# Optimization experiments

Measured on AMD Instinct MI355X. Metric: run time of the kernel, lower is better.

## Reference

```python
import jax, jax.numpy as jnp
import numpy as np
from jax import lax

TAGSET = 48
START_TAG = 46
STOP_TAG = 47
B, T = 128, 256

def setup_inputs() -> dict:
    key = jax.random.key(0)
    k1, k2, k3 = jax.random.split(key, 3)
    features = jax.random.normal(k1, (B, T, TAGSET, TAGSET), dtype=jnp.float32)
    targets = jax.random.randint(k2, (B, T), 0, TAGSET * TAGSET, dtype=jnp.int64)
    # lengths in [1, T], sorted descending as pack_padded_sequence expects
    lengths = jnp.sort(jax.random.randint(k3, (B,), 1, T + 1, dtype=jnp.int64))[::-1]
    return {"features": features, "targets": targets, "lengths": lengths}

def reference(features, targets, lengths):
    b, t, k, _ = features.shape
    # gold score: gather flattened (from_tag*K + to_tag) scores, sum over valid timesteps
    gathered = jnp.take_along_axis(
        features.reshape(b, t, k * k), targets[..., None], axis=2
    ).squeeze(-1)  # (B, T)
    valid = jnp.arange(t)[None, :] < lengths[:, None]  # (B, T) bool
    gold_score = jnp.sum(jnp.where(valid, gathered, 0.0))

    # forward algorithm: t=0 initializes from START_TAG row (all lengths >= 1)
    init = features[:, 0, START_TAG, :]  # (B, K)

    def step(scores_upto_t, inputs):
        feats_t, mask_t = inputs  # (B, K, K), (B,)
        upd = jax.nn.logsumexp(feats_t + scores_upto_t[:, :, None], axis=1)  # lse over from-tag
        new = jnp.where(mask_t[:, None], upd, scores_upto_t)  # freeze finished sequences
        return new, None

    feats_rest = jnp.swapaxes(features[:, 1:], 0, 1)  # (T-1, B, K, K)
    mask_rest = jnp.swapaxes(valid[:, 1:], 0, 1)      # (T-1, B)
    final, _ = lax.scan(step, init, (feats_rest, mask_rest))
    all_paths_scores = final[:, STOP_TAG].sum()
    return all_paths_scores - gold_score
```

## Files before the change

kernel.cpp:

```cpp
#include <hip/hip_runtime.h>


#define NB 128
#define NT 256
#define NK 48
#define NKK (NK * NK)
#define TAG_START 46
#define TAG_STOP 47
#define K_LOG2E 1.4426950408889634f
#define K_LN2   0.6931471805599453f

#define DECL48(v) \
  float v##0,v##1,v##2,v##3,v##4,v##5,v##6,v##7,v##8,v##9,v##10,v##11, \
        v##12,v##13,v##14,v##15,v##16,v##17,v##18,v##19,v##20,v##21,v##22,v##23, \
        v##24,v##25,v##26,v##27,v##28,v##29,v##30,v##31,v##32,v##33,v##34,v##35, \
        v##36,v##37,v##38,v##39,v##40,v##41,v##42,v##43,v##44,v##45,v##46,v##47;

#define LD48C(v, p) \
  v##0 =(p)[0*NK];  v##1 =(p)[1*NK];  v##2 =(p)[2*NK];  v##3 =(p)[3*NK]; \
  v##4 =(p)[4*NK];  v##5 =(p)[5*NK];  v##6 =(p)[6*NK];  v##7 =(p)[7*NK]; \
  v##8 =(p)[8*NK];  v##9 =(p)[9*NK];  v##10=(p)[10*NK]; v##11=(p)[11*NK]; \
  v##12=(p)[12*NK]; v##13=(p)[13*NK]; v##14=(p)[14*NK]; v##15=(p)[15*NK]; \
  v##16=(p)[16*NK]; v##17=(p)[17*NK]; v##18=(p)[18*NK]; v##19=(p)[19*NK]; \
  v##20=(p)[20*NK]; v##21=(p)[21*NK]; v##22=(p)[22*NK]; v##23=(p)[23*NK]; \
  v##24=(p)[24*NK]; v##25=(p)[25*NK]; v##26=(p)[26*NK]; v##27=(p)[27*NK]; \
  v##28=(p)[28*NK]; v##29=(p)[29*NK]; v##30=(p)[30*NK]; v##31=(p)[31*NK]; \
  v##32=(p)[32*NK]; v##33=(p)[33*NK]; v##34=(p)[34*NK]; v##35=(p)[35*NK]; \
  v##36=(p)[36*NK]; v##37=(p)[37*NK]; v##38=(p)[38*NK]; v##39=(p)[39*NK]; \
  v##40=(p)[40*NK]; v##41=(p)[41*NK]; v##42=(p)[42*NK]; v##43=(p)[43*NK]; \
  v##44=(p)[44*NK]; v##45=(p)[45*NK]; v##46=(p)[46*NK]; v##47=(p)[47*NK];

#define LD48R(v, p) { \
  const float4* q_ = (const float4*)(p); \
  float4 r0_=q_[0], r1_=q_[1], r2_ =q_[2],  r3_ =q_[3]; \
  float4 r4_=q_[4], r5_=q_[5], r6_ =q_[6],  r7_ =q_[7]; \
  float4 r8_=q_[8], r9_=q_[9], r10_=q_[10], r11_=q_[11]; \
  v##0 =r0_.x;  v##1 =r0_.y;  v##2 =r0_.z;  v##3 =r0_.w; \
  v##4 =r1_.x;  v##5 =r1_.y;  v##6 =r1_.z;  v##7 =r1_.w; \
  v##8 =r2_.x;  v##9 =r2_.y;  v##10=r2_.z;  v##11=r2_.w; \
  v##12=r3_.x;  v##13=r3_.y;  v##14=r3_.z;  v##15=r3_.w; \
  v##16=r4_.x;  v##17=r4_.y;  v##18=r4_.z;  v##19=r4_.w; \
  v##20=r5_.x;  v##21=r5_.y;  v##22=r5_.z;  v##23=r5_.w; \
  v##24=r6_.x;  v##25=r6_.y;  v##26=r6_.z;  v##27=r6_.w; \
  v##28=r7_.x;  v##29=r7_.y;  v##30=r7_.z;  v##31=r7_.w; \
  v##32=r8_.x;  v##33=r8_.y;  v##34=r8_.z;  v##35=r8_.w; \
  v##36=r9_.x;  v##37=r9_.y;  v##38=r9_.z;  v##39=r9_.w; \
  v##40=r10_.x; v##41=r10_.y; v##42=r10_.z; v##43=r10_.w; \
  v##44=r11_.x; v##45=r11_.y; v##46=r11_.z; v##47=r11_.w; }

#define RL(i) __int_as_float(__builtin_amdgcn_readlane(__float_as_int(s2), (i)))
#define TT(v,i) exp2f(__builtin_fmaf(v##i, K_LOG2E, RL(i)))

#define SUMTREE48(v) \
 ((((((TT(v,0)+TT(v,1))+(TT(v,2)+TT(v,3)))+((TT(v,4)+TT(v,5))+(TT(v,6)+TT(v,7)))) + \
    (((TT(v,8)+TT(v,9))+(TT(v,10)+TT(v,11)))+((TT(v,12)+TT(v,13))+(TT(v,14)+TT(v,15))))) + \
   ((((TT(v,16)+TT(v,17))+(TT(v,18)+TT(v,19)))+((TT(v,20)+TT(v,21))+(TT(v,22)+TT(v,23)))) + \
    (((TT(v,24)+TT(v,25))+(TT(v,26)+TT(v,27)))+((TT(v,28)+TT(v,29))+(TT(v,30)+TT(v,31)))))) + \
  ((((TT(v,32)+TT(v,33))+(TT(v,34)+TT(v,35)))+((TT(v,36)+TT(v,37))+(TT(v,38)+TT(v,39)))) + \
   (((TT(v,40)+TT(v,41))+(TT(v,42)+TT(v,43)))+((TT(v,44)+TT(v,45))+(TT(v,46)+TT(v,47))))))

#define STEP48(v, LDM) { \
  float acc_ = SUMTREE48(v); \
  { int up_ = u + 3; if (up_ > nsteps) up_ = nsteps; \
    const float* p_ = basep + (long)up_ * dstep; LDM(v, p_) } \
  float l2_ = __log2f(acc_); \
  float d2_ = __int_as_float(__builtin_amdgcn_readfirstlane(__float_as_int(l2_))); \
  s2 = l2_ - d2_; \
  c  = __builtin_fmaf(d2_, K_LN2, c); \
}

#define CHAIN48(LDM) { \
  DECL48(A) DECL48(B) DECL48(C) \
  { const float* p_ = basep + dstep; LDM(A, p_) } \
  { int up_ = (2 > nsteps) ? nsteps : 2; \
    const float* p_ = basep + (long)up_ * dstep; LDM(B, p_) } \
  { int up_ = (3 > nsteps) ? nsteps : 3; \
    const float* p_ = basep + (long)up_ * dstep; LDM(C, p_) } \
  int u = 1; \
  for (;;) { \
    STEP48(A, LDM) if (++u > nsteps) break; \
    STEP48(B, LDM) if (++u > nsteps) break; \
    STEP48(C, LDM) if (++u > nsteps) break; \
  } \
}

__global__ __launch_bounds__(64, 1)
void viterbi_chain_kernel(const float* __restrict__ feats,
                          const int* __restrict__ targets,
                          const int* __restrict__ lengths,
                          float* __restrict__ out,
                          float* __restrict__ ws)
{
    const int bu   = blockIdx.x;
    const int b    = bu >> 1;
    const int dir  = bu & 1;
    const int lane = threadIdx.x;
    const int len = lengths[b], last = len - 1, m = last >> 1;
    const float* __restrict__ fb = feats + (size_t)b * (NT * NKK);

    float gold = 0.f;
    {
        int t   = dir ? (m + 1 + lane) : lane;
        int tmx = dir ? last : m;
        while (t <= tmx) { gold += fb[(size_t)t * NKK + targets[b * NT + t]]; t += 64; }
        #pragma unroll
        for (int o = 32; o; o >>= 1) gold += __shfl_down(gold, o, 64);
    }

    const int ooc = (lane < NK) ? lane : (NK - 1);
    int nsteps = dir ? (last - 1 - m) : m;
    if (nsteps < 0) nsteps = 0;

    float s2, c = 0.f;
    if (dir) s2 = (last == 0) ? ((ooc == TAG_STOP) ? 0.f : -1e30f)
                              : fb[(size_t)last * NKK + (size_t)ooc * NK + TAG_STOP] * K_LOG2E;
    else     s2 = fb[TAG_START * NK + ooc] * K_LOG2E;

    if (nsteps > 0) {
        if (dir) {
            const float* basep = fb + (size_t)last * NKK + (size_t)ooc * NK;
            const long dstep = -(long)NKK;
            CHAIN48(LD48R)
        } else {
            const float* basep = fb + ooc;
            const long dstep = (long)NKK;
            CHAIN48(LD48C)
        }
    }

    if (lane < NK) ws[(size_t)bu * 64 + lane] = s2 * K_LN2;
    if (lane == 0) {
        ws[(size_t)bu * 64 + 48] = c;
        atomicAdd(out, -gold);
    }
}

__global__ __launch_bounds__(64, 1)
void viterbi_combine_kernel(const float* __restrict__ ws,
                            float* __restrict__ out)
{
    const int b = blockIdx.x, lane = threadIdx.x;
    const float* f = ws + (size_t)(2 * b) * 64;
    const float* g = ws + (size_t)(2 * b + 1) * 64;
    float v = -3.0e38f;
    if (lane < NK) v = f[lane] + g[lane];
    float mm = v;
    #pragma unroll
    for (int o = 32; o; o >>= 1) mm = fmaxf(mm, __shfl_xor(mm, o, 64));
    float e = (lane < NK) ? __expf(v - mm) : 0.f;
    #pragma unroll
    for (int o = 32; o; o >>= 1) e += __shfl_xor(e, o, 64);
    if (lane == 0) atomicAdd(out, __logf(e) + mm + f[NK] + g[NK]);
}

extern "C" void kernel_launch(void* const* d_in, const int* in_sizes, int n_in,
                              void* d_out, int out_size, void* d_ws, size_t ws_size,
                              hipStream_t stream) {
    const float* feats   = (const float*)d_in[0];
    const int*   targets = (const int*)d_in[1];
    const int*   lengths = (const int*)d_in[2];
    float*       out     = (float*)d_out;
    float*       ws      = (float*)d_ws;

    hipMemsetAsync(out, 0, sizeof(float), stream);
    viterbi_chain_kernel<<<dim3(2 * NB), dim3(64), 0, stream>>>(feats, targets, lengths, out, ws);
    viterbi_combine_kernel<<<dim3(NB), dim3(64), 0, stream>>>(ws, out);
}
```

Measured before the change: 506.9 us.

## Stage forward-direction step matrices through LDS with coalesced float4 loads

In the forward chain, each lane used to load a strided column of 48 floats per step. Now the whole wave loads each 48x48 step matrix with coalesced float4 loads, prefetched several steps ahead in registers, and writes it into a double-buffered shared-memory tile. The logsumexp then reads its column from LDS. The change also adds scheduling barriers and swaps exp2f for the AMDGCN exp2 builtin. This aims to cut uncoalesced global traffic, but LDS writes and reads now sit on the serial critical path of each step, and there is no explicit barrier between writing and reading the tile (a single wave, so it is likely safe).

```diff
diff --git a/kernel.cpp b/kernel.cpp
--- a/kernel.cpp
+++ b/kernel.cpp
@@ -10,25 +10,21 @@
 #define K_LOG2E 1.4426950408889634f
 #define K_LN2   0.6931471805599453f
 
+#if __has_builtin(__builtin_amdgcn_exp2f)
+#define EXP2(x) __builtin_amdgcn_exp2f(x)
+#else
+#define EXP2(x) exp2f(x)
+#endif
+
+#define SB() __builtin_amdgcn_sched_barrier(0)
+
+#define RL(i) __int_as_float(__builtin_amdgcn_readlane(__float_as_int(s2), (i)))
+
 #define DECL48(v) \
   float v##0,v##1,v##2,v##3,v##4,v##5,v##6,v##7,v##8,v##9,v##10,v##11, \
         v##12,v##13,v##14,v##15,v##16,v##17,v##18,v##19,v##20,v##21,v##22,v##23, \
         v##24,v##25,v##26,v##27,v##28,v##29,v##30,v##31,v##32,v##33,v##34,v##35, \
         v##36,v##37,v##38,v##39,v##40,v##41,v##42,v##43,v##44,v##45,v##46,v##47;
-
-#define LD48C(v, p) \
-  v##0 =(p)[0*NK];  v##1 =(p)[1*NK];  v##2 =(p)[2*NK];  v##3 =(p)[3*NK]; \
-  v##4 =(p)[4*NK];  v##5 =(p)[5*NK];  v##6 =(p)[6*NK];  v##7 =(p)[7*NK]; \
-  v##8 =(p)[8*NK];  v##9 =(p)[9*NK];  v##10=(p)[10*NK]; v##11=(p)[11*NK]; \
-  v##12=(p)[12*NK]; v##13=(p)[13*NK]; v##14=(p)[14*NK]; v##15=(p)[15*NK]; \
-  v##16=(p)[16*NK]; v##17=(p)[17*NK]; v##18=(p)[18*NK]; v##19=(p)[19*NK]; \
-  v##20=(p)[20*NK]; v##21=(p)[21*NK]; v##22=(p)[22*NK]; v##23=(p)[23*NK]; \
-  v##24=(p)[24*NK]; v##25=(p)[25*NK]; v##26=(p)[26*NK]; v##27=(p)[27*NK]; \
-  v##28=(p)[28*NK]; v##29=(p)[29*NK]; v##30=(p)[30*NK]; v##31=(p)[31*NK]; \
-  v##32=(p)[32*NK]; v##33=(p)[33*NK]; v##34=(p)[34*NK]; v##35=(p)[35*NK]; \
-  v##36=(p)[36*NK]; v##37=(p)[37*NK]; v##38=(p)[38*NK]; v##39=(p)[39*NK]; \
-  v##40=(p)[40*NK]; v##41=(p)[41*NK]; v##42=(p)[42*NK]; v##43=(p)[43*NK]; \
-  v##44=(p)[44*NK]; v##45=(p)[45*NK]; v##46=(p)[46*NK]; v##47=(p)[47*NK];
 
 #define LD48R(v, p) { \
   const float4* q_ = (const float4*)(p); \
@@ -48,8 +44,7 @@
   v##40=r10_.x; v##41=r10_.y; v##42=r10_.z; v##43=r10_.w; \
   v##44=r11_.x; v##45=r11_.y; v##46=r11_.z; v##47=r11_.w; }
 
-#define RL(i) __int_as_float(__builtin_amdgcn_readlane(__float_as_int(s2), (i)))
-#define TT(v,i) exp2f(__builtin_fmaf(v##i, K_LOG2E, RL(i)))
+#define TT(v,i) EXP2(__builtin_fmaf(v##i, vlog2e, RL(i)))
 
 #define SUMTREE48(v) \
  ((((((TT(v,0)+TT(v,1))+(TT(v,2)+TT(v,3)))+((TT(v,4)+TT(v,5))+(TT(v,6)+TT(v,7)))) + \
@@ -59,29 +54,66 @@
   ((((TT(v,32)+TT(v,33))+(TT(v,34)+TT(v,35)))+((TT(v,36)+TT(v,37))+(TT(v,38)+TT(v,39)))) + \
    (((TT(v,40)+TT(v,41))+(TT(v,42)+TT(v,43)))+((TT(v,44)+TT(v,45))+(TT(v,46)+TT(v,47))))))
 
-#define STEP48(v, LDM) { \
+#define STEPB(v) { \
   float acc_ = SUMTREE48(v); \
   { int up_ = u + 3; if (up_ > nsteps) up_ = nsteps; \
-    const float* p_ = basep + (long)up_ * dstep; LDM(v, p_) } \
+    const float* p_ = basep + (long)up_ * dstep; LD48R(v, p_) } \
+  SB(); \
   float l2_ = __log2f(acc_); \
   float d2_ = __int_as_float(__builtin_amdgcn_readfirstlane(__float_as_int(l2_))); \
   s2 = l2_ - d2_; \
   c  = __builtin_fmaf(d2_, K_LN2, c); \
 }
 
-#define CHAIN48(LDM) { \
+#define CHAINB() { \
   DECL48(A) DECL48(B) DECL48(C) \
-  { const float* p_ = basep + dstep; LDM(A, p_) } \
+  { const float* p_ = basep + dstep; LD48R(A, p_) } \
   { int up_ = (2 > nsteps) ? nsteps : 2; \
-    const float* p_ = basep + (long)up_ * dstep; LDM(B, p_) } \
+    const float* p_ = basep + (long)up_ * dstep; LD48R(B, p_) } \
   { int up_ = (3 > nsteps) ? nsteps : 3; \
-    const float* p_ = basep + (long)up_ * dstep; LDM(C, p_) } \
+    const float* p_ = basep + (long)up_ * dstep; LD48R(C, p_) } \
   int u = 1; \
   for (;;) { \
-    STEP48(A, LDM) if (++u > nsteps) break; \
-    STEP48(B, LDM) if (++u > nsteps) break; \
-    STEP48(C, LDM) if (++u > nsteps) break; \
+    STEPB(A) if (++u > nsteps) break; \
+    STEPB(B) if (++u > nsteps) break; \
+    STEPB(C) if (++u > nsteps) break; \
   } \
+}
+
+#define DECL9(R) float4 R##0,R##1,R##2,R##3,R##4,R##5,R##6,R##7,R##8;
+
+#define GLD9(R, base) { const float4* q_ = (const float4*)(base); \
+  R##0=q_[lane];     R##1=q_[lane+64];  R##2=q_[lane+128]; \
+  R##3=q_[lane+192]; R##4=q_[lane+256]; R##5=q_[lane+320]; \
+  R##6=q_[lane+384]; R##7=q_[lane+448]; R##8=q_[lane+512]; }
+
+#define WRT9(R, tb) { float4* w_ = (float4*)(tb); \
+  w_[lane]=R##0;     w_[lane+64]=R##1;  w_[lane+128]=R##2; \
+  w_[lane+192]=R##3; w_[lane+256]=R##4; w_[lane+320]=R##5; \
+  w_[lane+384]=R##6; w_[lane+448]=R##7; w_[lane+512]=R##8; }
+
+#define FT(TBR,k) EXP2(__builtin_fmaf(TBF[TBR][k][jc], vlog2e, RL(k)))
+
+#define FSUM(TBR) \
+ ((((((FT(TBR,0)+FT(TBR,1))+(FT(TBR,2)+FT(TBR,3)))+((FT(TBR,4)+FT(TBR,5))+(FT(TBR,6)+FT(TBR,7)))) + \
+    (((FT(TBR,8)+FT(TBR,9))+(FT(TBR,10)+FT(TBR,11)))+((FT(TBR,12)+FT(TBR,13))+(FT(TBR,14)+FT(TBR,15))))) + \
+   ((((FT(TBR,16)+FT(TBR,17))+(FT(TBR,18)+FT(TBR,19)))+((FT(TBR,20)+FT(TBR,21))+(FT(TBR,22)+FT(TBR,23)))) + \
+    (((FT(TBR,24)+FT(TBR,25))+(FT(TBR,26)+FT(TBR,27)))+((FT(TBR,28)+FT(TBR,29))+(FT(TBR,30)+FT(TBR,31)))))) + \
+  ((((FT(TBR,32)+FT(TBR,33))+(FT(TBR,34)+FT(TBR,35)))+((FT(TBR,36)+FT(TBR,37))+(FT(TBR,38)+FT(TBR,39)))) + \
+   (((FT(TBR,40)+FT(TBR,41))+(FT(TBR,42)+FT(TBR,43)))+((FT(TBR,44)+FT(TBR,45))+(FT(TBR,46)+FT(TBR,47))))))
+
+#define STEPF(Ri, Rw, TBR, TBW) { \
+  { int up_ = u + 3; if (up_ > nsteps) up_ = nsteps; \
+    GLD9(Ri, fb + (size_t)up_ * NKK) } \
+  SB(); \
+  float acc_ = FSUM(TBR); \
+  SB(); \
+  WRT9(Rw, TBF[TBW]) \
+  SB(); \
+  float l2_ = __log2f(acc_); \
+  float d2_ = __int_as_float(__builtin_amdgcn_readfirstlane(__float_as_int(l2_))); \
+  s2 = l2_ - d2_; \
+  c  = __builtin_fmaf(d2_, K_LN2, c); \
 }
 
 __global__ __launch_bounds__(64, 1)
@@ -97,6 +129,9 @@
     const int lane = threadIdx.x;
     const int len = lengths[b], last = len - 1, m = last >> 1;
     const float* __restrict__ fb = feats + (size_t)b * (NT * NKK);
+    const float vlog2e = K_LOG2E;
+
+    __shared__ __align__(16) float TBF[2][NK][NK];
 
     float gold = 0.f;
     {
@@ -108,6 +143,7 @@
     }
 
     const int ooc = (lane < NK) ? lane : (NK - 1);
+    const int jc  = ooc;
     int nsteps = dir ? (last - 1 - m) : m;
     if (nsteps < 0) nsteps = 0;
 
@@ -120,11 +156,22 @@
         if (dir) {
             const float* basep = fb + (size_t)last * NKK + (size_t)ooc * NK;
             const long dstep = -(long)NKK;
-            CHAIN48(LD48R)
+            CHAINB()
         } else {
-            const float* basep = fb + ooc;
-            const long dstep = (long)NKK;
-            CHAIN48(LD48C)
+            DECL9(R0f) DECL9(R1f) DECL9(R2f)
+            { int u_ = (1 > nsteps) ? nsteps : 1; GLD9(R1f, fb + (size_t)u_ * NKK) }
+            { int u_ = (2 > nsteps) ? nsteps : 2; GLD9(R2f, fb + (size_t)u_ * NKK) }
+            { int u_ = (3 > nsteps) ? nsteps : 3; GLD9(R0f, fb + (size_t)u_ * NKK) }
+            WRT9(R1f, TBF[1])
+            int u = 1;
+            for (;;) {
+                STEPF(R1f, R2f, 1, 0) if (++u > nsteps) break;
+                STEPF(R2f, R0f, 0, 1) if (++u > nsteps) break;
+                STEPF(R0f, R1f, 1, 0) if (++u > nsteps) break;
+                STEPF(R1f, R2f, 0, 1) if (++u > nsteps) break;
+                STEPF(R2f, R0f, 1, 0) if (++u > nsteps) break;
+                STEPF(R0f, R1f, 0, 1) if (++u > nsteps) break;
+            }
         }
     }
 
```

Result: faster. 426.5 us (-15.9%).
